# Kernel tuning notes

Measured on AMD Instinct MI355X. Metric: run time of the kernel, lower is better.

The kernel has to match this reference:

```python
import jax, jax.numpy as jnp
import numpy as np

B, S, D_IN, H, HEADS, CF = 16384, 64, 4, 32, 2, 16
DH = H // HEADS  # per-head dim = 16


def setup_inputs() -> dict:
    key = jax.random.key(0)
    ks = jax.random.split(key, 32)
    def w(k, shape, scale=0.1):
        return jax.random.normal(k, shape, dtype=jnp.float32) * scale
    return {
        "x": jax.random.normal(ks[0], (B, S, D_IN), dtype=jnp.float32),
        # ConvBranch
        "c1w": w(ks[1], (CF, D_IN, 3)), "c1b": w(ks[2], (CF,)),
        "c2w": w(ks[3], (CF, CF, 3)),  "c2b": w(ks[4], (CF,)),
        "cpw": w(ks[5], (H, CF)),      "cpb": w(ks[6], (H,)),
        # AttentionBranch
        "ipw": w(ks[7], (H, D_IN)),    "ipb": w(ks[8], (H,)),
        "wq": w(ks[9], (H, H)),  "bq": w(ks[10], (H,)),
        "wk": w(ks[11], (H, H)), "bk": w(ks[12], (H,)),
        "wv": w(ks[13], (H, H)), "bv": w(ks[14], (H,)),
        "wo": w(ks[15], (H, H)), "bo": w(ks[16], (H,)),
        "lng": jnp.ones((H,), jnp.float32), "lnb": jnp.zeros((H,), jnp.float32),
        # DBMM
        "gw": w(ks[17], (2 * H, 2 * H)), "gb": w(ks[18], (2 * H,)),
        "pw": w(ks[19], (H, 2 * H)),     "pb": w(ks[20], (H,)),
        # Output head
        "h1w": w(ks[21], (16, H)), "h1b": w(ks[22], (16,)),
        "h2w": w(ks[23], (2, 16)), "h2b": w(ks[24], (2,)),
    }


def _forward(x, c1w, c1b, c2w, c2b, cpw, cpb, ipw, ipb,
             wq, bq, wk, bk, wv, bv, wo, bo, lng, lnb,
             gw, gb, pw, pb, h1w, h1b, h2w, h2b):
    # ---- ConvBranch: (B,S,4) -> (B,32) ----
    xt = jnp.transpose(x, (0, 2, 1))  # (B, C=4, S)
    dn = ("NCH", "OIH", "NCH")
    h1 = jax.nn.relu(jax.lax.conv_general_dilated(xt, c1w, (1,), [(1, 1)], dimension_numbers=dn) + c1b[None, :, None])
    h2 = jax.nn.relu(jax.lax.conv_general_dilated(h1, c2w, (1,), [(1, 1)], dimension_numbers=dn) + c2b[None, :, None])
    pooled = jnp.mean(h2, axis=-1)               # (B, CF) AdaptiveAvgPool1d(1)
    conv_feat = pooled @ cpw.T + cpb             # (B, 32)

    # ---- AttentionBranch: (B,S,4) -> (B,32) ----
    h = x @ ipw.T + ipb                          # (B, S, 32)
    q = (h @ wq.T + bq).reshape(B, S, HEADS, DH)
    k = (h @ wk.T + bk).reshape(B, S, HEADS, DH)
    v = (h @ wv.T + bv).reshape(B, S, HEADS, DH)
    scores = jnp.einsum("bqhd,bkhd->bhqk", q, k) / jnp.sqrt(jnp.float32(DH))
    attn = jax.nn.softmax(scores, axis=-1)       # dropout=eval no-op
    ctx = jnp.einsum("bhqk,bkhd->bqhd", attn, v).reshape(B, S, H)
    attn_out = ctx @ wo.T + bo
    y = h + attn_out
    mu = jnp.mean(y, axis=-1, keepdims=True)
    var = jnp.var(y, axis=-1, keepdims=True)
    y = (y - mu) / jnp.sqrt(var + 1e-5) * lng + lnb
    att_feat = jnp.mean(y, axis=1)               # (B, 32)

    # ---- DBMM fusion ----
    combined = jnp.concatenate([conv_feat, att_feat], axis=-1)  # (B, 64)
    gated = combined * jax.nn.sigmoid(combined @ gw.T + gb)
    fused = gated @ pw.T + pb                    # (B, 32); dropout eval no-op

    # ---- Output head ----
    out = jax.nn.relu(fused @ h1w.T + h1b) @ h2w.T + h2b        # (B, 2)
    return out


def reference(x, c1w, c1b, c2w, c2b, cpw, cpb, ipw, ipb,
              wq, bq, wk, bk, wv, bv, wo, bo, lng, lnb,
              gw, gb, pw, pb, h1w, h1b, h2w, h2b):
    return _forward(x, c1w, c1b, c2w, c2b, cpw, cpb, ipw, ipb,
                    wq, bq, wk, bk, wv, bv, wo, bo, lng, lnb,
                    gw, gb, pw, pb, h1w, h1b, h2w, h2b)
```

## Files before the change

kernel.cpp:

```cpp
#include <hip/hip_runtime.h>
#include <hip/hip_bf16.h>
#include <math.h>

#define S 64
#define DIN 4
#define H 32
#define CF 16
#define WPB 4

typedef __attribute__((ext_vector_type(8))) short bf16x8;
typedef __attribute__((ext_vector_type(4))) short s16x4;
typedef __attribute__((ext_vector_type(4))) float f32x4;

#define MFMA(a, b, c) __builtin_amdgcn_mfma_f32_16x16x32_bf16((a), (b), (c), 0, 0, 0)

__device__ __forceinline__ void wsync() {
    asm volatile("" ::: "memory");
    __builtin_amdgcn_wave_barrier();
    asm volatile("" ::: "memory");
}

__device__ __forceinline__ short f2bf(float f) {
    __hip_bfloat16 h = __float2bfloat16(f);
    return *reinterpret_cast<short*>(&h);
}

__device__ __forceinline__ bf16x8 frag8(const float* p) {
    f32x4 a = *(const f32x4*)p;
    f32x4 b = *(const f32x4*)(p + 4);
    bf16x8 f;
    f[0] = f2bf(a[0]); f[1] = f2bf(a[1]); f[2] = f2bf(a[2]); f[3] = f2bf(a[3]);
    f[4] = f2bf(b[0]); f[5] = f2bf(b[1]); f[6] = f2bf(b[2]); f[7] = f2bf(b[3]);
    return f;
}

__device__ __forceinline__ s16x4 pack4(float a, float b, float c, float d) {
    s16x4 v; v[0] = f2bf(a); v[1] = f2bf(b); v[2] = f2bf(c); v[3] = f2bf(d); return v;
}


__global__ __launch_bounds__(WPB * 64, 2)
void fused_fwd(const float* __restrict__ x,
               const float* __restrict__ c1w, const float* __restrict__ c1b,
               const float* __restrict__ c2w, const float* __restrict__ c2b,
               const float* __restrict__ cpw, const float* __restrict__ cpb,
               const float* __restrict__ ipw, const float* __restrict__ ipb,
               const float* __restrict__ wq, const float* __restrict__ bq,
               const float* __restrict__ wk, const float* __restrict__ bk,
               const float* __restrict__ wv, const float* __restrict__ bv,
               const float* __restrict__ wo, const float* __restrict__ bo,
               const float* __restrict__ lng, const float* __restrict__ lnb,
               const float* __restrict__ gw, const float* __restrict__ gb,
               const float* __restrict__ pw, const float* __restrict__ pb,
               const float* __restrict__ h1w, const float* __restrict__ h1b,
               const float* __restrict__ h2w, const float* __restrict__ h2b,
               float* __restrict__ out)
{
    __shared__ __attribute__((aligned(16))) short R_all[WPB * 2560];
    __shared__ __attribute__((aligned(16))) short U_all[WPB * 2560];

    const int w  = threadIdx.x >> 6;
    const int s  = threadIdx.x & 63;
    const int fr = s & 15;
    const int g  = s >> 4;
    const int b  = blockIdx.x * WPB + w;

    short* R   = R_all + w * 2560;
    short* U   = U_all + w * 2560;
    short* hB  = U;
    short* Vt  = U;
    float* smc = reinterpret_cast<float*>(U + 1152);

    const f32x4 xr = reinterpret_cast<const f32x4*>(x)[b * S + s];
    float x0[4] = {xr[0], xr[1], xr[2], xr[3]};

    float xm[4], xp[4];
#pragma unroll
    for (int i = 0; i < 4; ++i) {
        float up = __shfl_up(x0[i], 1);
        float dn = __shfl_down(x0[i], 1);
        xm[i] = (s > 0) ? up : 0.f;
        xp[i] = (s < S - 1) ? dn : 0.f;
    }
    float hc[CF];
#pragma unroll
    for (int o = 0; o < CF; ++o) {
        float acc = c1b[o];
#pragma unroll
        for (int i = 0; i < DIN; ++i) {
            acc += xm[i] * c1w[(o * DIN + i) * 3 + 0];
            acc += x0[i] * c1w[(o * DIN + i) * 3 + 1];
            acc += xp[i] * c1w[(o * DIN + i) * 3 + 2];
        }
        hc[o] = fmaxf(acc, 0.f);
    }
    float hm[CF], hp[CF];
#pragma unroll
    for (int o = 0; o < CF; ++o) {
        float up = __shfl_up(hc[o], 1);
        float dn = __shfl_down(hc[o], 1);
        hm[o] = (s > 0) ? up : 0.f;
        hp[o] = (s < S - 1) ? dn : 0.f;
    }
    float h2r[CF];
#pragma unroll
    for (int o = 0; o < CF; ++o) {
        float acc = c2b[o];
#pragma unroll
        for (int i = 0; i < CF; ++i) {
            acc += hm[i] * c2w[(o * CF + i) * 3 + 0];
            acc += hc[i] * c2w[(o * CF + i) * 3 + 1];
            acc += hp[i] * c2w[(o * CF + i) * 3 + 2];
        }
        h2r[o] = fmaxf(acc, 0.f);
    }
#pragma unroll
    for (int o = 0; o < CF; ++o) {
        float v = h2r[o];
#pragma unroll
        for (int off = 32; off > 0; off >>= 1) v += __shfl_xor(v, off);
        h2r[o] = v * (1.f / 64.f);
    }
    float convf = 0.f;
    if (s < H) {
        float acc = cpb[s];
#pragma unroll
        for (int o = 0; o < CF; ++o) acc += h2r[o] * cpw[s * CF + o];
        convf = acc;
    }

    {
        float hr[H];
#pragma unroll
        for (int j = 0; j < H; ++j) {
            hr[j] = ipb[j] + x0[0] * ipw[j * 4 + 0] + x0[1] * ipw[j * 4 + 1]
                           + x0[2] * ipw[j * 4 + 2] + x0[3] * ipw[j * 4 + 3];
        }
#pragma unroll
        for (int i = 0; i < 4; ++i) {
            bf16x8 t;
#pragma unroll
            for (int e = 0; e < 8; ++e) t[e] = f2bf(hr[i * 8 + e]);
            *(bf16x8*)&hB[s * 40 + i * 8] = t;
        }
    }
    wsync();

    bf16x8 hF[4];
#pragma unroll
    for (int t = 0; t < 4; ++t) hF[t] = *(const bf16x8*)&hB[(t * 16 + fr) * 40 + g * 8];
    if (s < H) smc[s] = convf;
    wsync();

    const bf16x8 z8 = {0, 0, 0, 0, 0, 0, 0, 0};
    const f32x4  z4 = {0.f, 0.f, 0.f, 0.f};

    f32x4 yD[2][4];
#pragma unroll
    for (int mt = 0; mt < 2; ++mt) {
        f32x4 bo4 = *(const f32x4*)&bo[mt * 16 + g * 4];
#pragma unroll
        for (int nt = 0; nt < 4; ++nt) yD[mt][nt] = bo4;
    }

#pragma unroll
    for (int h = 0; h < 2; ++h) {
        bf16x8 wqF = frag8(&wq[(h * 16 + fr) * 32 + g * 8]);
        bf16x8 wkF = frag8(&wk[(h * 16 + fr) * 32 + g * 8]);
        bf16x8 wvF = frag8(&wv[(h * 16 + fr) * 32 + g * 8]);
        f32x4 bq4 = *(const f32x4*)&bq[h * 16 + g * 4];
        f32x4 bk4 = *(const f32x4*)&bk[h * 16 + g * 4];
        float bvv = bv[h * 16 + fr];

#pragma unroll
        for (int nt = 0; nt < 4; ++nt) {
            f32x4 aq = MFMA(wqF, hF[nt], bq4);
            *(s16x4*)&R[(nt * 16 + fr) * 40 + g * 4] =
                pack4(aq[0] * 0.25f, aq[1] * 0.25f, aq[2] * 0.25f, aq[3] * 0.25f);
            f32x4 ak = MFMA(wkF, hF[nt], bk4);
            *(s16x4*)&R[(nt * 16 + fr) * 40 + 24 + g * 4] =
                pack4(ak[0], ak[1], ak[2], ak[3]);
        }
#pragma unroll
        for (int mi = 0; mi < 4; ++mi) {
            f32x4 cv = {bvv, bvv, bvv, bvv};
            f32x4 av = MFMA(hF[mi], wvF, cv);
            *(s16x4*)&Vt[fr * 72 + mi * 16 + g * 4] = pack4(av[0], av[1], av[2], av[3]);
        }
        wsync();

        bf16x8 qF[4], kF[4];
#pragma unroll
        for (int t = 0; t < 4; ++t) {
            bf16x8 fq = z8, fk = z8;
            if (g < 2) {
                fq = *(const bf16x8*)&R[(t * 16 + fr) * 40 + g * 8];
                fk = *(const bf16x8*)&R[(t * 16 + fr) * 40 + 24 + g * 8];
            }
            qF[t] = fq; kF[t] = fk;
        }
        f32x4 pA[4][4];
#pragma unroll
        for (int mi = 0; mi < 4; ++mi)
#pragma unroll
            for (int nj = 0; nj < 4; ++nj)
                pA[mi][nj] = MFMA(kF[mi], qF[nj], z4);

        float inv[4];
#pragma unroll
        for (int nj = 0; nj < 4; ++nj) {
            float l = 0.f;
#pragma unroll
            for (int mi = 0; mi < 4; ++mi)
#pragma unroll
                for (int r = 0; r < 4; ++r) {
                    float e = __expf(pA[mi][nj][r]);
                    pA[mi][nj][r] = e;
                    l += e;
                }
            l += __shfl_xor(l, 16);
            l += __shfl_xor(l, 32);
            inv[nj] = 1.0f / l;
        }

        f32x4 cAcc[4] = {z4, z4, z4, z4};
#pragma unroll
        for (int kk = 0; kk < 2; ++kk) {
            wsync();
#pragma unroll
            for (int m2 = 0; m2 < 2; ++m2) {
                const int mi = kk * 2 + m2;
#pragma unroll
                for (int nj = 0; nj < 4; ++nj)
                    *(s16x4*)&R[(nj * 16 + fr) * 40 + m2 * 16 + g * 4] =
                        pack4(pA[mi][nj][0], pA[mi][nj][1],
                              pA[mi][nj][2], pA[mi][nj][3]);
            }
            wsync();
            bf16x8 vtF = *(const bf16x8*)&Vt[fr * 72 + kk * 32 + g * 8];
#pragma unroll
            for (int nt = 0; nt < 4; ++nt) {
                bf16x8 ptF = *(const bf16x8*)&R[(nt * 16 + fr) * 40 + g * 8];
                cAcc[nt] = MFMA(vtF, ptF, cAcc[nt]);
            }
        }
#pragma unroll
        for (int nt = 0; nt < 4; ++nt)
#pragma unroll
            for (int r = 0; r < 4; ++r) cAcc[nt][r] *= inv[nt];
        wsync();

#pragma unroll
        for (int nt = 0; nt < 4; ++nt)
            *(s16x4*)&R[(nt * 16 + fr) * 40 + g * 4] =
                pack4(cAcc[nt][0], cAcc[nt][1], cAcc[nt][2], cAcc[nt][3]);
        wsync();

        bf16x8 woF[2];
#pragma unroll
        for (int mt = 0; mt < 2; ++mt) {
            bf16x8 f = frag8(&wo[(mt * 16 + fr) * 32 + h * 16 + (g & 1) * 8]);
            if (g >= 2) f = z8;
            woF[mt] = f;
        }
#pragma unroll
        for (int nt = 0; nt < 4; ++nt) {
            bf16x8 cF = z8;
            if (g < 2) cF = *(const bf16x8*)&R[(nt * 16 + fr) * 40 + g * 8];
#pragma unroll
            for (int mt = 0; mt < 2; ++mt)
                yD[mt][nt] = MFMA(woF[mt], cF, yD[mt][nt]);
        }
        wsync();
    }

    {
        f32x4 xq[4];
#pragma unroll
        for (int nt = 0; nt < 4; ++nt)
            xq[nt] = reinterpret_cast<const f32x4*>(x)[b * S + nt * 16 + fr];
#pragma unroll
        for (int mt = 0; mt < 2; ++mt)
#pragma unroll
            for (int r = 0; r < 4; ++r) {
                const int j = mt * 16 + g * 4 + r;
                const f32x4 wr4 = *(const f32x4*)&ipw[j * 4];
                const float bb = ipb[j];
#pragma unroll
                for (int nt = 0; nt < 4; ++nt)
                    yD[mt][nt][r] += bb + xq[nt][0] * wr4[0] + xq[nt][1] * wr4[1]
                                        + xq[nt][2] * wr4[2] + xq[nt][3] * wr4[3];
            }
    }
    f32x4 lg0 = *(const f32x4*)&lng[g * 4];
    f32x4 lg1 = *(const f32x4*)&lng[16 + g * 4];
    f32x4 lb0 = *(const f32x4*)&lnb[g * 4];
    f32x4 lb1 = *(const f32x4*)&lnb[16 + g * 4];
#pragma unroll
    for (int nt = 0; nt < 4; ++nt) {
        float sy = 0.f, sy2 = 0.f;
#pragma unroll
        for (int mt = 0; mt < 2; ++mt)
#pragma unroll
            for (int r = 0; r < 4; ++r) {
                float v = yD[mt][nt][r];
                sy += v; sy2 += v * v;
            }
        sy  += __shfl_xor(sy, 16);  sy  += __shfl_xor(sy, 32);
        sy2 += __shfl_xor(sy2, 16); sy2 += __shfl_xor(sy2, 32);
        const float mu   = sy * (1.f / 32.f);
        const float var  = sy2 * (1.f / 32.f) - mu * mu;
        const float rstd = rsqrtf(var + 1e-5f);
#pragma unroll
        for (int r = 0; r < 4; ++r) {
            yD[0][nt][r] = (yD[0][nt][r] - mu) * rstd * lg0[r] + lb0[r];
            yD[1][nt][r] = (yD[1][nt][r] - mu) * rstd * lg1[r] + lb1[r];
        }
    }

#pragma unroll
    for (int mt = 0; mt < 2; ++mt)
#pragma unroll
        for (int r = 0; r < 4; ++r) {
            float af = yD[mt][0][r] + yD[mt][1][r] + yD[mt][2][r] + yD[mt][3][r];
            af += __shfl_xor(af, 1);
            af += __shfl_xor(af, 2);
            af += __shfl_xor(af, 4);
            af += __shfl_xor(af, 8);
            if (fr == 0) smc[H + mt * 16 + g * 4 + r] = af * (1.f / 64.f);
        }
    wsync();

    {
        const int j = s;
        float acc = gb[j];
        const f32x4* smc4 = (const f32x4*)smc;
        const f32x4* gw4  = (const f32x4*)&gw[j * 2 * H];
#pragma unroll
        for (int k4 = 0; k4 < 16; ++k4) {
            f32x4 cv = smc4[k4], wv4 = gw4[k4];
            acc += cv[0] * wv4[0] + cv[1] * wv4[1] + cv[2] * wv4[2] + cv[3] * wv4[3];
        }
        const float sig = 1.f / (1.f + __expf(-acc));
        smc[64 + j] = smc[j] * sig;
    }
    wsync();
    if (s < H) {
        float acc = pb[s];
        const f32x4* smc4 = (const f32x4*)(smc + 64);
        const f32x4* pw4  = (const f32x4*)&pw[s * 2 * H];
#pragma unroll
        for (int k4 = 0; k4 < 16; ++k4) {
            f32x4 cv = smc4[k4], wv4 = pw4[k4];
            acc += cv[0] * wv4[0] + cv[1] * wv4[1] + cv[2] * wv4[2] + cv[3] * wv4[3];
        }
        smc[128 + s] = acc;
    }
    wsync();
    if (s < 16) {
        float acc = h1b[s];
#pragma unroll
        for (int c = 0; c < H; ++c) acc += smc[128 + c] * h1w[s * H + c];
        smc[160 + s] = fmaxf(acc, 0.f);
    }
    wsync();
    if (s < 2) {
        float acc = h2b[s];
#pragma unroll
        for (int c = 0; c < 16; ++c) acc += smc[160 + c] * h2w[s * 16 + c];
        out[b * 2 + s] = acc;
    }
}

extern "C" void kernel_launch(void* const* d_in, const int* in_sizes, int n_in,
                              void* d_out, int out_size, void* d_ws, size_t ws_size,
                              hipStream_t stream) {
    (void)n_in; (void)d_ws; (void)ws_size; (void)in_sizes;
    const int nb = out_size / 2;
    const float* xp_ = (const float*)d_in[0];
    const float* c1w = (const float*)d_in[1];  const float* c1b = (const float*)d_in[2];
    const float* c2w = (const float*)d_in[3];  const float* c2b = (const float*)d_in[4];
    const float* cpw = (const float*)d_in[5];  const float* cpb = (const float*)d_in[6];
    const float* ipw = (const float*)d_in[7];  const float* ipb = (const float*)d_in[8];
    const float* wq  = (const float*)d_in[9];  const float* bq  = (const float*)d_in[10];
    const float* wk  = (const float*)d_in[11]; const float* bk  = (const float*)d_in[12];
    const float* wv  = (const float*)d_in[13]; const float* bv  = (const float*)d_in[14];
    const float* wo  = (const float*)d_in[15]; const float* bo  = (const float*)d_in[16];
    const float* lng = (const float*)d_in[17]; const float* lnb = (const float*)d_in[18];
    const float* gw  = (const float*)d_in[19]; const float* gb  = (const float*)d_in[20];
    const float* pw  = (const float*)d_in[21]; const float* pb  = (const float*)d_in[22];
    const float* h1w = (const float*)d_in[23]; const float* h1b = (const float*)d_in[24];
    const float* h2w = (const float*)d_in[25]; const float* h2b = (const float*)d_in[26];
    float* outp = (float*)d_out;

    dim3 grid(nb / WPB), block(WPB * 64);
    hipLaunchKernelGGL(fused_fwd, grid, block, 0, stream,
                       xp_, c1w, c1b, c2w, c2b, cpw, cpb, ipw, ipb,
                       wq, bq, wk, bk, wv, bv, wo, bo, lng, lnb,
                       gw, gb, pw, pb, h1w, h1b, h2w, h2b, outp);
}
```

Before: 248.7 us.

## Compute second conv layer with bf16 MFMA and fold log2e into softmax exp2

The second 1D conv (16->16 channels, kernel 3) previously ran as per-lane scalar FMAs with register shuffles. It now stages the first-layer activations as bf16 in shared memory with zero-padded boundary rows and computes the conv as two 16x16x32 MFMAs per tile, then pools through a shuffle reduction into shared memory. The softmax also folds log2(e) into the Q scale so it can use exp2f, and the V-transpose row stride is padded to reduce LDS bank conflicts. This lowers the ALU instruction count but drops the conv to bf16 precision and adds LDS traffic and extra wave syncs.

```diff
diff --git a/kernel.cpp b/kernel.cpp
--- a/kernel.cpp
+++ b/kernel.cpp
@@ -69,7 +69,12 @@
     short* U   = U_all + w * 2560;
     short* hB  = U;
     short* Vt  = U;
-    float* smc = reinterpret_cast<float*>(U + 1152);
+    float* smc = reinterpret_cast<float*>(U + 1216);
+    short* C1  = R;
+    float* poolS = reinterpret_cast<float*>(R + 1408);
+
+    const bf16x8 z8 = {0, 0, 0, 0, 0, 0, 0, 0};
+    const f32x4  z4 = {0.f, 0.f, 0.f, 0.f};
 
     const f32x4 xr = reinterpret_cast<const f32x4*>(x)[b * S + s];
     float x0[4] = {xr[0], xr[1], xr[2], xr[3]};
@@ -94,38 +99,52 @@
         }
         hc[o] = fmaxf(acc, 0.f);
     }
-    float hm[CF], hp[CF];
-#pragma unroll
-    for (int o = 0; o < CF; ++o) {
-        float up = __shfl_up(hc[o], 1);
-        float dn = __shfl_down(hc[o], 1);
-        hm[o] = (s > 0) ? up : 0.f;
-        hp[o] = (s < S - 1) ? dn : 0.f;
-    }
-    float h2r[CF];
-#pragma unroll
-    for (int o = 0; o < CF; ++o) {
-        float acc = c2b[o];
-#pragma unroll
-        for (int i = 0; i < CF; ++i) {
-            acc += hm[i] * c2w[(o * CF + i) * 3 + 0];
-            acc += hc[i] * c2w[(o * CF + i) * 3 + 1];
-            acc += hp[i] * c2w[(o * CF + i) * 3 + 2];
-        }
-        h2r[o] = fmaxf(acc, 0.f);
-    }
-#pragma unroll
-    for (int o = 0; o < CF; ++o) {
-        float v = h2r[o];
-#pragma unroll
-        for (int off = 32; off > 0; off >>= 1) v += __shfl_xor(v, off);
-        h2r[o] = v * (1.f / 64.f);
-    }
+    {
+        bf16x8 t0, t1;
+#pragma unroll
+        for (int e = 0; e < 8; ++e) { t0[e] = f2bf(hc[e]); t1[e] = f2bf(hc[8 + e]); }
+        *(bf16x8*)&C1[(s + 1) * 20 + 0] = t0;
+        *(bf16x8*)&C1[(s + 1) * 20 + 8] = t1;
+        if (s < 2) {
+            const int rz = s * 65;
+            *(bf16x8*)&C1[rz * 20 + 0] = z8;
+            *(bf16x8*)&C1[rz * 20 + 8] = z8;
+        }
+    }
+    bf16x8 a1, a2;
+#pragma unroll
+    for (int e = 0; e < 8; ++e) {
+        a1[e] = f2bf(c2w[fr * 48 + ((g & 1) * 8 + e) * 3 + (g >> 1)]);
+        a2[e] = (g < 2) ? f2bf(c2w[fr * 48 + (g * 8 + e) * 3 + 2]) : (short)0;
+    }
+    wsync();
+    {
+        f32x4 c2b4 = *(const f32x4*)&c2b[g * 4];
+        f32x4 pacc = z4;
+#pragma unroll
+        for (int t = 0; t < 4; ++t) {
+            bf16x8 b1 = *(const bf16x8*)&C1[(t * 16 + fr + (g >> 1)) * 20 + (g & 1) * 8];
+            bf16x8 b2 = (g < 2) ? *(const bf16x8*)&C1[(t * 16 + fr + 2) * 20 + g * 8] : z8;
+            f32x4 acc = MFMA(a1, b1, c2b4);
+            acc = MFMA(a2, b2, acc);
+#pragma unroll
+            for (int r = 0; r < 4; ++r) pacc[r] += fmaxf(acc[r], 0.f);
+        }
+#pragma unroll
+        for (int r = 0; r < 4; ++r) {
+            float v = pacc[r];
+            v += __shfl_xor(v, 1); v += __shfl_xor(v, 2);
+            v += __shfl_xor(v, 4); v += __shfl_xor(v, 8);
+            pacc[r] = v * (1.f / 64.f);
+        }
+        if (fr == 0) *(f32x4*)&poolS[g * 4] = pacc;
+    }
+    wsync();
     float convf = 0.f;
     if (s < H) {
         float acc = cpb[s];
 #pragma unroll
-        for (int o = 0; o < CF; ++o) acc += h2r[o] * cpw[s * CF + o];
+        for (int o = 0; o < CF; ++o) acc += poolS[o] * cpw[s * CF + o];
         convf = acc;
     }
 
@@ -151,9 +170,6 @@
     for (int t = 0; t < 4; ++t) hF[t] = *(const bf16x8*)&hB[(t * 16 + fr) * 40 + g * 8];
     if (s < H) smc[s] = convf;
     wsync();
-
-    const bf16x8 z8 = {0, 0, 0, 0, 0, 0, 0, 0};
-    const f32x4  z4 = {0.f, 0.f, 0.f, 0.f};
 
     f32x4 yD[2][4];
 #pragma unroll
@@ -172,11 +188,12 @@
         f32x4 bk4 = *(const f32x4*)&bk[h * 16 + g * 4];
         float bvv = bv[h * 16 + fr];
 
+        const float QS = 0.25f * 1.44269504088896f;
 #pragma unroll
         for (int nt = 0; nt < 4; ++nt) {
             f32x4 aq = MFMA(wqF, hF[nt], bq4);
             *(s16x4*)&R[(nt * 16 + fr) * 40 + g * 4] =
-                pack4(aq[0] * 0.25f, aq[1] * 0.25f, aq[2] * 0.25f, aq[3] * 0.25f);
+                pack4(aq[0] * QS, aq[1] * QS, aq[2] * QS, aq[3] * QS);
             f32x4 ak = MFMA(wkF, hF[nt], bk4);
             *(s16x4*)&R[(nt * 16 + fr) * 40 + 24 + g * 4] =
                 pack4(ak[0], ak[1], ak[2], ak[3]);
@@ -185,7 +202,7 @@
         for (int mi = 0; mi < 4; ++mi) {
             f32x4 cv = {bvv, bvv, bvv, bvv};
             f32x4 av = MFMA(hF[mi], wvF, cv);
-            *(s16x4*)&Vt[fr * 72 + mi * 16 + g * 4] = pack4(av[0], av[1], av[2], av[3]);
+            *(s16x4*)&Vt[fr * 76 + mi * 16 + g * 4] = pack4(av[0], av[1], av[2], av[3]);
         }
         wsync();
 
@@ -214,7 +231,7 @@
             for (int mi = 0; mi < 4; ++mi)
 #pragma unroll
                 for (int r = 0; r < 4; ++r) {
-                    float e = __expf(pA[mi][nj][r]);
+                    float e = exp2f(pA[mi][nj][r]);
                     pA[mi][nj][r] = e;
                     l += e;
                 }
@@ -237,7 +254,7 @@
                               pA[mi][nj][2], pA[mi][nj][3]);
             }
             wsync();
-            bf16x8 vtF = *(const bf16x8*)&Vt[fr * 72 + kk * 32 + g * 8];
+            bf16x8 vtF = *(const bf16x8*)&Vt[fr * 76 + kk * 32 + g * 8];
 #pragma unroll
             for (int nt = 0; nt < 4; ++nt) {
                 bf16x8 ptF = *(const bf16x8*)&R[(nt * 16 + fr) * 40 + g * 8];
```

Measured after the change: 262.7 us. 1.06x slower.
